# Performance work log

Measured on AMD Instinct MI355X. Metric: run time of the kernel, lower is better.

Reference implementation:

```python
import jax, jax.numpy as jnp
import numpy as np
from jax import lax

B, S, D, H, HFF, T = 256, 33, 42, 128, 256, 20
BN_EPS = 1e-5

def _bn(x, g, b):
    # eval-mode BatchNorm1d with running_mean=0, running_var=1
    return x * (g / jnp.sqrt(1.0 + BN_EPS)) + b

def _gelu(x):
    return jax.nn.gelu(x, approximate=False)  # torch default GELU (exact)

def setup_inputs() -> dict:
    key = jax.random.key(0)
    ks = iter(jax.random.split(key, 48))
    w = lambda shp, s=0.02: jax.random.normal(next(ks), shp, dtype=jnp.float32) * s
    z = lambda shp: jnp.zeros(shp, jnp.float32)
    o = lambda shp: jnp.ones(shp, jnp.float32)
    inp = {
        'interaction_path': jax.random.normal(next(ks), (B, S, D), dtype=jnp.float32),
        'timestamps': jnp.broadcast_to(jnp.arange(S, dtype=jnp.float32) * 0.1, (B, S)),
        # initial encoder: Linear(42->128), BN, GELU, Linear(128->128), BN
        'enc_w1': w((D, H)), 'enc_b1': z(H), 'enc_g1': o(H), 'enc_be1': z(H),
        'enc_w2': w((H, H)), 'enc_b2': z(H), 'enc_g2': o(H), 'enc_be2': z(H),
        # vector field: 128->256 (BN,GELU), 256->256 (BN,GELU) x2, 256->5376
        'vf_w0': w((H, HFF)), 'vf_b0': z(HFF), 'vf_g0': o(HFF), 'vf_be0': z(HFF),
        'vf_w1': w((HFF, HFF)), 'vf_b1': z(HFF), 'vf_g1': o(HFF), 'vf_be1': z(HFF),
        'vf_w2': w((HFF, HFF)), 'vf_b2': z(HFF), 'vf_g2': o(HFF), 'vf_be2': z(HFF),
        'vf_w3': w((HFF, H * D)), 'vf_b3': z(H * D),
        # multihead attention (seq_len = 1 -> softmax is identically 1)
        'wv': w((H, H)), 'bv': z(H), 'wo': w((H, H)), 'bo': z(H),
        # 20 trait decoders, stacked: 128->64->32->1
        'dw1': w((T, H, 64)), 'db1': z((T, 64)),
        'dw2': w((T, 64, 32)), 'db2': z((T, 32)),
        'dw3': w((T, 32, 1)), 'db3': z((T, 1)),
    }
    return inp

def reference(interaction_path, timestamps,
              enc_w1, enc_b1, enc_g1, enc_be1, enc_w2, enc_b2, enc_g2, enc_be2,
              vf_w0, vf_b0, vf_g0, vf_be0, vf_w1, vf_b1, vf_g1, vf_be1,
              vf_w2, vf_b2, vf_g2, vf_be2, vf_w3, vf_b3,
              wv, bv, wo, bo,
              dw1, db1, dw2, db2, dw3, db3):
    b = interaction_path.shape[0]
    # ---- initial encoder on X[:, 0] ----
    x0 = interaction_path[:, 0]                      # [B, D]
    h = _gelu(_bn(x0 @ enc_w1 + enc_b1, enc_g1, enc_be1))
    z0 = _bn(h @ enc_w2 + enc_b2, enc_g2, enc_be2)   # [B, H]

    # ---- CDE vector field: z -> [B, H, D] ----
    def vf(zz):
        y = _gelu(_bn(zz @ vf_w0 + vf_b0, vf_g0, vf_be0))
        y = _gelu(_bn(y @ vf_w1 + vf_b1, vf_g1, vf_be1))
        y = _gelu(_bn(y @ vf_w2 + vf_b2, vf_g2, vf_be2))
        return (y @ vf_w3 + vf_b3).reshape(b, H, D)

    def g(zz, dxdt):  # f(z) @ dX/dt  -> [B, H]
        return jnp.einsum('bhd,bd->bh', vf(zz), dxdt)

    # linear-interpolation control path: piecewise-constant derivative
    t = timestamps[0]                                # [S]
    dt = t[1:] - t[:-1]                              # [S-1]
    dX = interaction_path[:, 1:] - interaction_path[:, :-1]   # [B, S-1, D]
    dXdt = dX / dt[None, :, None]                    # [B, S-1, D]

    def step(zz, x):
        dxdt, hstep = x
        k1 = g(zz, dxdt)
        k2 = g(zz + 0.5 * hstep * k1, dxdt)
        k3 = g(zz + 0.5 * hstep * k2, dxdt)
        k4 = g(zz + hstep * k3, dxdt)
        return zz + (hstep / 6.0) * (k1 + 2.0 * k2 + 2.0 * k3 + k4), None

    zT, _ = lax.scan(step, z0, (jnp.swapaxes(dXdt, 0, 1), dt))  # [B, H]

    # ---- self-attention over a length-1 sequence: softmax==1 -> out_proj(v) ----
    attended = (zT @ wv + bv) @ wo + bo              # [B, H]

    # ---- 20 trait decoders (stacked / vectorized) ----
    h1 = _gelu(jnp.einsum('bh,thd->tbd', attended, dw1) + db1[:, None, :])
    h2 = _gelu(jnp.einsum('tbd,tde->tbe', h1, dw2) + db2[:, None, :])
    out = jax.nn.sigmoid(jnp.einsum('tbe,teo->tbo', h2, dw3) + db3[:, None, :])
    return jnp.transpose(out[..., 0], (1, 0))        # [B, 20]
```

## Files before the change

kernel.cpp:

```cpp
#include <hip/hip_runtime.h>
#include <cstdint>

constexpr int B    = 256;
constexpr int S    = 33;
constexpr int D    = 42;
constexpr int H    = 128;
constexpr int HFF  = 256;
constexpr int T    = 20;
constexpr int NSTEP = S - 1;
constexpr int DP   = D / 2;
constexpr int ADW  = 8192;
constexpr int CH   = 16;
constexpr int NCH  = NSTEP / CH;
#define BN_SCALE 0.9999950000374997f

typedef _Float16 h2v __attribute__((ext_vector_type(2)));
typedef _Float16 f16x8 __attribute__((ext_vector_type(8)));
typedef float    f32x4 __attribute__((ext_vector_type(4)));
union UH2 { uint32_t u; h2v h; };

__device__ __forceinline__ float fdot2u(uint32_t a, uint32_t b, float c) {
    UH2 x, y; x.u = a; y.u = b;
    return __builtin_amdgcn_fdot2(x.h, y.h, c, false);
}
__device__ __forceinline__ uint32_t packh2(float a, float b) {
    UH2 u; u.h = h2v{(_Float16)a, (_Float16)b}; return u.u;
}
__device__ __forceinline__ float gelu_exact(float x) {
    return 0.5f * x * (1.0f + erff(x * 0.70710678118654752f));
}
__device__ __forceinline__ float gelu_fast(float x) {
    float inner = x * (1.0f + 0.044715f * x * x);
    float E = __expf(1.5957691216f * inner);
    return x * E * __frcp_rn(E + 1.0f);
}
__device__ __forceinline__ int aswz(int idx) {
    return (idx & ~31) | ((idx & 31) ^ (((idx >> 9) & 3) << 1));
}

__global__ void __launch_bounds__(256) packprep_kernel(
    const float* __restrict__ w0, const float* __restrict__ w1,
    const float* __restrict__ w2, const float* __restrict__ w3,
    uint32_t* __restrict__ wcol, uint32_t* __restrict__ wp,
    const float* __restrict__ path, const float* __restrict__ ts,
    const float* __restrict__ ew1, const float* __restrict__ eb1,
    const float* __restrict__ eg1, const float* __restrict__ ebe1,
    const float* __restrict__ ew2, const float* __restrict__ eb2,
    const float* __restrict__ eg2, const float* __restrict__ ebe2,
    const float* __restrict__ b3,
    float* __restrict__ zbuf, uint32_t* __restrict__ dxp,
    float* __restrict__ bd3g, float* __restrict__ dtb) {
    int tid = threadIdx.x;
    if (blockIdx.x < 4096) {
        int idx = blockIdx.x * 256 + tid;
        if (idx < 160 * 512) {
            int r = idx >> 9, t = idx & 511;
            int j = t >> 1, half = t & 1;
            float a, bb;
            if (r < 32)      { int ip = half * 32 + r;      a = w0[(2*ip)*HFF + j]; bb = w0[(2*ip+1)*HFF + j]; }
            else if (r < 96) { int ip = half * 64 + (r-32); a = w1[(2*ip)*HFF + j]; bb = w1[(2*ip+1)*HFF + j]; }
            else             { int ip = half * 64 + (r-96); a = w2[(2*ip)*HFF + j]; bb = w2[(2*ip+1)*HFF + j]; }
            wcol[idx] = packh2(a, bb);
        }
        if (idx < 32768 * 32) {
            int m = idx >> 5, dd = (idx & 31) * 2;
            int e = 4 * (m >> 9) + (m & 3);
            int h = (m >> 2) & 127;
            const float* row = w3 + (size_t)e * (H * D) + h * D;
            float a = (dd     < D) ? row[dd]     : 0.f;
            float b = (dd + 1 < D) ? row[dd + 1] : 0.f;
            wp[idx] = packh2(a, b);
        }
        return;
    }
    __shared__ float x0[D], hb[H], dxs[NSTEP][D];
    int b = blockIdx.x - 4096;
    if (tid < D) x0[tid] = path[b * S * D + tid];
    __syncthreads();
    if (tid < H) {
        float acc = eb1[tid];
        for (int d = 0; d < D; ++d) acc += x0[d] * ew1[d * H + tid];
        hb[tid] = gelu_exact(acc * (eg1[tid] * BN_SCALE) + ebe1[tid]);
    }
    __syncthreads();
    if (tid < H) {
        float acc = eb2[tid];
        for (int i = 0; i < H; ++i) acc += hb[i] * ew2[i * H + tid];
        zbuf[b * H + tid] = acc * (eg2[tid] * BN_SCALE) + ebe2[tid];
    }
    for (int idx = tid; idx < NSTEP * 32; idx += 256) {
        int s = idx >> 5, j2 = idx & 31;
        uint32_t val = 0;
        if (j2 < DP) {
            float dtv = ts[s + 1] - ts[s];
            int base = b * S * D + s * D + 2 * j2;
            float v0 = (path[base + D] - path[base]) / dtv;
            float v1 = (path[base + D + 1] - path[base + 1]) / dtv;
            dxs[s][2 * j2] = v0; dxs[s][2 * j2 + 1] = v1;
            val = packh2(v0, v1);
        }
        dxp[((size_t)(s * B + b)) * 32 + j2] = val;
    }
    __syncthreads();
    if (tid < H) {
        for (int s = 0; s < NSTEP; ++s) {
            float a = 0.f;
            for (int d = 0; d < D; ++d) a += b3[tid * D + d] * dxs[s][d];
            bd3g[(size_t)(s * B + b) * H + tid] = a;
        }
    }
    if (b == 0 && tid < NSTEP) dtb[tid] = ts[tid + 1] - ts[tid];
}

__global__ void __launch_bounds__(256) amm_kernel(
    const uint32_t* __restrict__ wp, const uint32_t* __restrict__ dxp,
    uint32_t* __restrict__ Ach, int s0) {
    __shared__ __align__(16) uint32_t xpose[4][16 * 36];
    int t = threadIdx.x;
    int l = t & 63, wid = t >> 6;
    int mg = (blockIdx.x & 63) * 4 + wid;
    int sg = blockIdx.x >> 6;
    int lr = l & 15, lk = l >> 4;
    const char* wpB = (const char*)wp;
    const char* dxB = (const char*)dxp + (size_t)s0 * B * 128;
    char* asB = (char*)Ach;
    uint32_t* xp = xpose[wid];
    f16x8 af0[8], af1[8];
#pragma unroll
    for (int mi = 0; mi < 8; ++mi) {
        const f16x8* p = (const f16x8*)(wpB + ((size_t)(mg * 8 + mi) * 16 + lr) * 128 + lk * 16);
        af0[mi] = p[0]; af1[mi] = p[4];
    }
#pragma unroll
    for (int si = 0; si < 8; ++si) {
        int q = sg * 128 + si * 16 + lr;
#pragma unroll
        for (int mi = 0; mi < 8; ++mi) {
            const f16x8* bp = (const f16x8*)(dxB + (size_t)q * 128 + lk * 16);
            f16x8 b0 = bp[0], b1 = bp[4];
            f32x4 acc = {0.f, 0.f, 0.f, 0.f};
            acc = __builtin_amdgcn_mfma_f32_16x16x32_f16(af0[mi], b0, acc, 0, 0, 0);
            acc = __builtin_amdgcn_mfma_f32_16x16x32_f16(af1[mi], b1, acc, 0, 0, 0);
            uint32_t P0 = packh2(acc[0], acc[1]) + 0x00800080u;
            uint32_t P1 = packh2(acc[2], acc[3]) + 0x00800080u;
            uint32_t Q = __builtin_amdgcn_perm(P1, P0, 0x07050301u);
            xp[lr * 36 + lk + 4 * mi] = Q;
        }
        __syncthreads();
        {
            int qr = l >> 2, seg = l & 3;
            const uint4* src = (const uint4*)(xp + qr * 36 + seg * 8);
            uint4 v0 = src[0], v1 = src[1];
            int qout = sg * 128 + si * 16 + qr;
            char* outB = asB + (size_t)qout * 32768 + mg * 128 + seg * 32;
            *(uint4*)outB = v0;
            *(uint4*)(outB + 16) = v1;
        }
        __syncthreads();
    }
}

__global__ void __launch_bounds__(512, 1)
__attribute__((amdgpu_waves_per_eu(2, 8)))
scan_kernel(
    const uint32_t* __restrict__ wcol, const uint32_t* __restrict__ Ach,
    const float* __restrict__ vb0, const float* __restrict__ vg0, const float* __restrict__ vbe0,
    const float* __restrict__ vb1, const float* __restrict__ vg1, const float* __restrict__ vbe1,
    const float* __restrict__ vb2, const float* __restrict__ vg2, const float* __restrict__ vbe2,
    const float* __restrict__ bd3g, const float* __restrict__ dtb,
    float* __restrict__ zbuf, int s0, int do_att,
    const float* __restrict__ wv, const float* __restrict__ bv,
    const float* __restrict__ wo, const float* __restrict__ bo,
    float* __restrict__ att) {
    __shared__ __align__(16) uint32_t ABUF[2][ADW];
    __shared__ __align__(16) uint32_t zzPd[72];
    __shared__ __align__(16) uint32_t yA[136], yB[136], yC[136];
    int t = threadIdx.x, b = blockIdx.x;
    int j = t >> 1, half = t & 1;
    int h = t >> 2, g = t & 3;
    int hswz = h ^ (g << 3);
    uint32_t w0h[32], w1h[64], w2h[64];
#pragma unroll
    for (int r = 0; r < 32; ++r) w0h[r] = wcol[r * 512 + t];
#pragma unroll
    for (int r = 0; r < 64; ++r) w1h[r] = wcol[(32 + r) * 512 + t];
#pragma unroll
    for (int r = 0; r < 64; ++r) w2h[r] = wcol[(96 + r) * 512 + t];
    float c0s = vg0[j] * BN_SCALE, c0o = vb0[j] * c0s + vbe0[j];
    float c1s = vg1[j] * BN_SCALE, c1o = vb1[j] * c1s + vbe1[j];
    float c2s = vg2[j] * BN_SCALE, c2o = vb2[j] * c2s + vbe2[j];
    float zf = zbuf[b * H + h];
    {
        const uint4* Ag = (const uint4*)(Ach + (size_t)b * ADW);
        uint4 a0 = Ag[t], a1 = Ag[512 + t], a2 = Ag[1024 + t], a3 = Ag[1536 + t];
        uint4* Ad = (uint4*)ABUF[0];
        Ad[aswz(t)] = a0; Ad[aswz(512 + t)] = a1;
        Ad[aswz(1024 + t)] = a2; Ad[aswz(1536 + t)] = a3;
    }
    {
        float zhi = __shfl_down(zf, 4, 64);
        if ((t & 7) == 0) {
            int ip = t >> 3;
            zzPd[(ip >> 5) * 36 + (ip & 31)] = packh2(zf, zhi);
        }
    }
    __syncthreads();

    for (int sl = 0; sl < CH; ++sl) {
        int s = s0 + sl;
        float hstep = dtb[s];
        float bd3 = bd3g[(size_t)(s * B + b) * H + h];
        uint4 pf0, pf1, pf2, pf3;
        {
            int sn = (sl + 1 < CH) ? sl + 1 : sl;
            const uint4* Ag = (const uint4*)(Ach + (size_t)(sn * B + b) * ADW);
            pf0 = Ag[t]; pf1 = Ag[512 + t]; pf2 = Ag[1024 + t]; pf3 = Ag[1536 + t];
        }
        const uint32_t* AL = ABUF[sl & 1];
        float ksum = 0.f, kcur = 0.f;
        for (int r = 0; r < 4; ++r) {
            {
                float pa = 0.f, pb = 0.f, pc = 0.f, pd = 0.f;
                const uint4* zq = (const uint4*)(zzPd + half * 36);
#pragma unroll
                for (int u4 = 0; u4 < 8; ++u4) {
                    uint4 zv = zq[u4];
                    pa = fdot2u(w0h[4*u4+0], zv.x, pa); pb = fdot2u(w0h[4*u4+1], zv.y, pb);
                    pc = fdot2u(w0h[4*u4+2], zv.z, pc); pd = fdot2u(w0h[4*u4+3], zv.w, pd);
                }
                float p = (pa + pb) + (pc + pd);
                p += __shfl_xor(p, 1, 64);
                float v = gelu_fast(p * c0s + c0o);
                float vhi = __shfl_down(v, 2, 64);
                if ((t & 3) == 0) {
                    int ip = t >> 2;
                    yA[(ip >> 6) * 68 + (ip & 63)] = packh2(v, vhi);
                }
            }
            __syncthreads();
            {
                float pa = 0.f, pb = 0.f, pc = 0.f, pd = 0.f;
                const uint4* yq = (const uint4*)(yA + half * 68);
#pragma unroll
                for (int u4 = 0; u4 < 16; ++u4) {
                    uint4 yv = yq[u4];
                    pa = fdot2u(w1h[4*u4+0], yv.x, pa); pb = fdot2u(w1h[4*u4+1], yv.y, pb);
                    pc = fdot2u(w1h[4*u4+2], yv.z, pc); pd = fdot2u(w1h[4*u4+3], yv.w, pd);
                }
                float p = (pa + pb) + (pc + pd);
                p += __shfl_xor(p, 1, 64);
                float v = gelu_fast(p * c1s + c1o);
                float vhi = __shfl_down(v, 2, 64);
                if ((t & 3) == 0) {
                    int ip = t >> 2;
                    yB[(ip >> 6) * 68 + (ip & 63)] = packh2(v, vhi);
                }
            }
            __syncthreads();
            {
                float pa = 0.f, pb = 0.f, pc = 0.f, pd = 0.f;
                const uint4* yq = (const uint4*)(yB + half * 68);
#pragma unroll
                for (int u4 = 0; u4 < 16; ++u4) {
                    uint4 yv = yq[u4];
                    pa = fdot2u(w2h[4*u4+0], yv.x, pa); pb = fdot2u(w2h[4*u4+1], yv.y, pb);
                    pc = fdot2u(w2h[4*u4+2], yv.z, pc); pd = fdot2u(w2h[4*u4+3], yv.w, pd);
                }
                float p = (pa + pb) + (pc + pd);
                p += __shfl_xor(p, 1, 64);
                float v = gelu_fast(p * c2s + c2o);
                float vhi = __shfl_down(v, 2, 64);
                if ((t & 3) == 0) {
                    int ip = t >> 2;
                    yC[(ip >> 6) * 68 + (ip & 63)] = packh2(v, vhi);
                }
            }
            __syncthreads();
            {
                float pA = 0.f, pB = 0.f, pC = 0.f, pD = 0.f;
                int ybase = (g >> 1) * 68 + (g & 1) * 32;
                const uint4* yq = (const uint4*)(yC + ybase);
#pragma unroll
                for (int kk = 0; kk < 8; ++kk) {
                    uint4 yv = yq[kk];
                    int k0 = g * 16 + 2 * kk;
                    uint32_t Qa = AL[k0 * 128 + hswz];
                    uint32_t Qb = AL[(k0 + 1) * 128 + hswz];
                    pA = fdot2u(__builtin_amdgcn_perm(0u, Qa, 0x010C000Cu), yv.x, pA);
                    pB = fdot2u(__builtin_amdgcn_perm(0u, Qa, 0x030C020Cu), yv.y, pB);
                    pC = fdot2u(__builtin_amdgcn_perm(0u, Qb, 0x010C000Cu), yv.z, pC);
                    pD = fdot2u(__builtin_amdgcn_perm(0u, Qb, 0x030C020Cu), yv.w, pD);
                }
                float ptot = (pA + pB) + (pC + pD);
                ptot += __shfl_xor(ptot, 1, 64);
                ptot += __shfl_xor(ptot, 2, 64);
                kcur = bd3 + ptot;
                float wsm = (r == 1 || r == 2) ? 2.f : 1.f;
                ksum += wsm * kcur;
                float zz;
                if (r < 3) {
                    float cin = (r == 2) ? 1.f : 0.5f;
                    zz = zf + cin * hstep * kcur;
                } else {
                    zf += hstep * (1.f / 6.f) * ksum;
                    zz = zf;
                }
                float zhi = __shfl_down(zz, 4, 64);
                if ((t & 7) == 0) {
                    int ip = t >> 3;
                    zzPd[(ip >> 5) * 36 + (ip & 31)] = packh2(zz, zhi);
                }
            }
            if (r == 3) {
                uint4* Ad = (uint4*)ABUF[(sl + 1) & 1];
                Ad[aswz(t)] = pf0; Ad[aswz(512 + t)] = pf1;
                Ad[aswz(1024 + t)] = pf2; Ad[aswz(1536 + t)] = pf3;
            }
            __syncthreads();
        }
    }
    if ((t & 3) == 0) zbuf[b * H + h] = zf;
    if (do_att) {
        float* zfl = (float*)ABUF[0];
        float* vv  = zfl + 128;
        if ((t & 3) == 0) zfl[h] = zf;
        __syncthreads();
        {
            float acc = 0.f;
            int i0 = 32 * g;
#pragma unroll 8
            for (int i = 0; i < 32; ++i) {
                int ii = i0 + ((i + 8 * g) & 31);
                acc += zfl[ii] * wv[ii * H + h];
            }
            acc += __shfl_xor(acc, 1, 64);
            acc += __shfl_xor(acc, 2, 64);
            if (g == 0) vv[h] = acc + bv[h];
        }
        __syncthreads();
        {
            float acc = 0.f;
            int i0 = 32 * g;
#pragma unroll 8
            for (int i = 0; i < 32; ++i) {
                int ii = i0 + ((i + 8 * g) & 31);
                acc += vv[ii] * wo[ii * H + h];
            }
            acc += __shfl_xor(acc, 1, 64);
            acc += __shfl_xor(acc, 2, 64);
            if (g == 0) att[b * H + h] = acc + bo[h];
        }
    }
}

__global__ void __launch_bounds__(64) dec_kernel(
    const float* __restrict__ att,
    const float* __restrict__ dw1, const float* __restrict__ db1,
    const float* __restrict__ dw2, const float* __restrict__ db2,
    const float* __restrict__ dw3, const float* __restrict__ db3,
    float* __restrict__ out) {
    int bid = blockIdx.x;
    int t = bid >> 8, b = bid & 255;
    int tid = threadIdx.x;
    __shared__ float al[H], h1l[64];
    al[tid] = att[b * H + tid];
    al[tid + 64] = att[b * H + tid + 64];
    __syncthreads();
    {
        float acc = db1[t * 64 + tid];
#pragma unroll 8
        for (int i = 0; i < H; ++i) acc += al[i] * dw1[t * H * 64 + i * 64 + tid];
        h1l[tid] = gelu_exact(acc);
    }
    __syncthreads();
    float v = 0.f;
    if (tid < 32) {
        float acc = db2[t * 32 + tid];
#pragma unroll 8
        for (int i = 0; i < 64; ++i) acc += h1l[i] * dw2[t * 64 * 32 + i * 32 + tid];
        v = gelu_exact(acc) * dw3[t * 32 + tid];
    }
#pragma unroll
    for (int off = 16; off >= 1; off >>= 1) v += __shfl_down(v, off, 64);
    if (tid == 0) out[b * T + t] = 1.f / (1.f + expf(-(v + db3[t])));
}

extern "C" void kernel_launch(void* const* d_in, const int* in_sizes, int n_in,
                              void* d_out, int out_size, void* d_ws, size_t ws_size,
                              hipStream_t stream) {
    const float* path = (const float*)d_in[0];
    const float* ts   = (const float*)d_in[1];
    const float* ew1  = (const float*)d_in[2];
    const float* eb1  = (const float*)d_in[3];
    const float* eg1  = (const float*)d_in[4];
    const float* ebe1 = (const float*)d_in[5];
    const float* ew2  = (const float*)d_in[6];
    const float* eb2  = (const float*)d_in[7];
    const float* eg2  = (const float*)d_in[8];
    const float* ebe2 = (const float*)d_in[9];
    const float* vw0  = (const float*)d_in[10];
    const float* vb0  = (const float*)d_in[11];
    const float* vg0  = (const float*)d_in[12];
    const float* vbe0 = (const float*)d_in[13];
    const float* vw1  = (const float*)d_in[14];
    const float* vb1  = (const float*)d_in[15];
    const float* vg1  = (const float*)d_in[16];
    const float* vbe1 = (const float*)d_in[17];
    const float* vw2  = (const float*)d_in[18];
    const float* vb2  = (const float*)d_in[19];
    const float* vg2  = (const float*)d_in[20];
    const float* vbe2 = (const float*)d_in[21];
    const float* vw3  = (const float*)d_in[22];
    const float* vb3  = (const float*)d_in[23];
    const float* wv   = (const float*)d_in[24];
    const float* bv   = (const float*)d_in[25];
    const float* wo   = (const float*)d_in[26];
    const float* bo   = (const float*)d_in[27];
    const float* dw1  = (const float*)d_in[28];
    const float* db1  = (const float*)d_in[29];
    const float* dw2  = (const float*)d_in[30];
    const float* db2  = (const float*)d_in[31];
    const float* dw3  = (const float*)d_in[32];
    const float* db3  = (const float*)d_in[33];

    char* ws = (char*)d_ws;
    size_t off = 0;
    auto take = [&](size_t bytes) { char* p = ws + off; off += (bytes + 255) & ~(size_t)255; return p; };
    uint32_t* Ach   = (uint32_t*)take((size_t)CH * B * ADW * 4);
    uint32_t* dxp   = (uint32_t*)take((size_t)NSTEP * B * 32 * 4);
    float*    bd3g  = (float*)take((size_t)NSTEP * B * H * 4);
    float*    dtb   = (float*)take(NSTEP * 4);
    float*    zbuf  = (float*)take((size_t)B * H * 4);
    float*    att   = (float*)take((size_t)B * H * 4);
    uint32_t* wcol  = (uint32_t*)take((size_t)160 * 512 * 4);
    uint32_t* wp    = (uint32_t*)take((size_t)32768 * 32 * 4);

    packprep_kernel<<<4096 + B, 256, 0, stream>>>(
        vw0, vw1, vw2, vw3, wcol, wp,
        path, ts, ew1, eb1, eg1, ebe1, ew2, eb2, eg2, ebe2, vb3,
        zbuf, dxp, bd3g, dtb);
    for (int c = 0; c < NCH; ++c) {
        amm_kernel<<<2048, 256, 0, stream>>>(wp, dxp, Ach, c * CH);
        scan_kernel<<<B, 512, 0, stream>>>(wcol, Ach,
                                           vb0, vg0, vbe0, vb1, vg1, vbe1, vb2, vg2, vbe2,
                                           bd3g, dtb, zbuf, c * CH,
                                           (c == NCH - 1) ? 1 : 0,
                                           wv, bv, wo, bo, att);
    }
    dec_kernel<<<T * B, 64, 0, stream>>>(att, dw1, db1, dw2, db2, dw3, db3, (float*)d_out);
}
```

Before: 532.5 us.

## Overlap next-chunk A-matrix GEMM with scan via fused double-buffered kernel

New measurement: 567.5 us. +6.6%, slower.

```diff
diff --git a/kernel.cpp b/kernel.cpp
--- a/kernel.cpp
+++ b/kernel.cpp
@@ -10,7 +10,7 @@
 constexpr int NSTEP = S - 1;
 constexpr int DP   = D / 2;
 constexpr int ADW  = 8192;
-constexpr int CH   = 16;
+constexpr int CH   = 8;
 constexpr int NCH  = NSTEP / CH;
 #define BN_SCALE 0.9999950000374997f
 
@@ -160,22 +160,74 @@
     }
 }
 
+template<int MODE>
 __global__ void __launch_bounds__(512, 1)
 __attribute__((amdgpu_waves_per_eu(2, 8)))
-scan_kernel(
-    const uint32_t* __restrict__ wcol, const uint32_t* __restrict__ Ach,
+scanx_kernel(
+    const uint32_t* __restrict__ wcol, const uint32_t* __restrict__ AchR,
+    uint32_t* __restrict__ AchW,
+    const uint32_t* __restrict__ wp, const uint32_t* __restrict__ dxp,
     const float* __restrict__ vb0, const float* __restrict__ vg0, const float* __restrict__ vbe0,
     const float* __restrict__ vb1, const float* __restrict__ vg1, const float* __restrict__ vbe1,
     const float* __restrict__ vb2, const float* __restrict__ vg2, const float* __restrict__ vbe2,
     const float* __restrict__ bd3g, const float* __restrict__ dtb,
-    float* __restrict__ zbuf, int s0, int do_att,
+    float* __restrict__ zbuf, int s0, int s0_amm,
     const float* __restrict__ wv, const float* __restrict__ bv,
     const float* __restrict__ wo, const float* __restrict__ bo,
     float* __restrict__ att) {
     __shared__ __align__(16) uint32_t ABUF[2][ADW];
     __shared__ __align__(16) uint32_t zzPd[72];
     __shared__ __align__(16) uint32_t yA[136], yB[136], yC[136];
-    int t = threadIdx.x, b = blockIdx.x;
+    int t = threadIdx.x;
+
+    if (MODE == 0 && blockIdx.x >= B) {
+        int rid = blockIdx.x - B;
+        int wid = t >> 6, l = t & 63;
+        int w = rid * 8 + wid;
+        int mg = w & 255, sg = w >> 8;
+        int lr = l & 15, lk = l >> 4;
+        const char* wpB = (const char*)wp;
+        const char* dxB = (const char*)dxp + (size_t)s0_amm * B * 128;
+        char* asB = (char*)AchW;
+        uint32_t* xp = (uint32_t*)ABUF[0] + wid * (16 * 36);
+        f16x8 af0[8], af1[8];
+#pragma unroll
+        for (int mi = 0; mi < 8; ++mi) {
+            const f16x8* p = (const f16x8*)(wpB + ((size_t)(mg * 8 + mi) * 16 + lr) * 128 + lk * 16);
+            af0[mi] = p[0]; af1[mi] = p[4];
+        }
+#pragma unroll
+        for (int si = 0; si < 8; ++si) {
+            int q = sg * 128 + si * 16 + lr;
+#pragma unroll
+            for (int mi = 0; mi < 8; ++mi) {
+                const f16x8* bp = (const f16x8*)(dxB + (size_t)q * 128 + lk * 16);
+                f16x8 b0 = bp[0], b1 = bp[4];
+                f32x4 acc = {0.f, 0.f, 0.f, 0.f};
+                acc = __builtin_amdgcn_mfma_f32_16x16x32_f16(af0[mi], b0, acc, 0, 0, 0);
+                acc = __builtin_amdgcn_mfma_f32_16x16x32_f16(af1[mi], b1, acc, 0, 0, 0);
+                uint32_t P0 = packh2(acc[0], acc[1]) + 0x00800080u;
+                uint32_t P1 = packh2(acc[2], acc[3]) + 0x00800080u;
+                uint32_t Q = __builtin_amdgcn_perm(P1, P0, 0x07050301u);
+                xp[lr * 36 + lk + 4 * mi] = Q;
+            }
+            __syncthreads();
+            {
+                int qr = l >> 2, seg = l & 3;
+                const uint4* src = (const uint4*)(xp + qr * 36 + seg * 8);
+                uint4 v0 = src[0], v1 = src[1];
+                int qout = sg * 128 + si * 16 + qr;
+                char* outB = asB + (size_t)qout * 32768 + mg * 128 + seg * 32;
+                *(uint4*)outB = v0;
+                *(uint4*)(outB + 16) = v1;
+            }
+            __syncthreads();
+        }
+        return;
+    }
+
+    __builtin_amdgcn_s_setprio(1);
+    int b = blockIdx.x;
     int j = t >> 1, half = t & 1;
     int h = t >> 2, g = t & 3;
     int hswz = h ^ (g << 3);
@@ -191,7 +243,7 @@
     float c2s = vg2[j] * BN_SCALE, c2o = vb2[j] * c2s + vbe2[j];
     float zf = zbuf[b * H + h];
     {
-        const uint4* Ag = (const uint4*)(Ach + (size_t)b * ADW);
+        const uint4* Ag = (const uint4*)(AchR + (size_t)b * ADW);
         uint4 a0 = Ag[t], a1 = Ag[512 + t], a2 = Ag[1024 + t], a3 = Ag[1536 + t];
         uint4* Ad = (uint4*)ABUF[0];
         Ad[aswz(t)] = a0; Ad[aswz(512 + t)] = a1;
@@ -213,7 +265,7 @@
         uint4 pf0, pf1, pf2, pf3;
         {
             int sn = (sl + 1 < CH) ? sl + 1 : sl;
-            const uint4* Ag = (const uint4*)(Ach + (size_t)(sn * B + b) * ADW);
+            const uint4* Ag = (const uint4*)(AchR + (size_t)(sn * B + b) * ADW);
             pf0 = Ag[t]; pf1 = Ag[512 + t]; pf2 = Ag[1024 + t]; pf3 = Ag[1536 + t];
         }
         const uint32_t* AL = ABUF[sl & 1];
@@ -320,7 +372,7 @@
         }
     }
     if ((t & 3) == 0) zbuf[b * H + h] = zf;
-    if (do_att) {
+    if (MODE == 1) {
         float* zfl = (float*)ABUF[0];
         float* vv  = zfl + 128;
         if ((t & 3) == 0) zfl[h] = zf;
@@ -426,7 +478,8 @@
     char* ws = (char*)d_ws;
     size_t off = 0;
     auto take = [&](size_t bytes) { char* p = ws + off; off += (bytes + 255) & ~(size_t)255; return p; };
-    uint32_t* Ach   = (uint32_t*)take((size_t)CH * B * ADW * 4);
+    uint32_t* Ach0  = (uint32_t*)take((size_t)CH * B * ADW * 4);
+    uint32_t* Ach1  = (uint32_t*)take((size_t)CH * B * ADW * 4);
     uint32_t* dxp   = (uint32_t*)take((size_t)NSTEP * B * 32 * 4);
     float*    bd3g  = (float*)take((size_t)NSTEP * B * H * 4);
     float*    dtb   = (float*)take(NSTEP * 4);
@@ -434,18 +487,27 @@
     float*    att   = (float*)take((size_t)B * H * 4);
     uint32_t* wcol  = (uint32_t*)take((size_t)160 * 512 * 4);
     uint32_t* wp    = (uint32_t*)take((size_t)32768 * 32 * 4);
+    uint32_t* AchB[2] = { Ach0, Ach1 };
 
     packprep_kernel<<<4096 + B, 256, 0, stream>>>(
         vw0, vw1, vw2, vw3, wcol, wp,
         path, ts, ew1, eb1, eg1, ebe1, ew2, eb2, eg2, ebe2, vb3,
         zbuf, dxp, bd3g, dtb);
+    amm_kernel<<<1024, 256, 0, stream>>>(wp, dxp, AchB[0], 0);
     for (int c = 0; c < NCH; ++c) {
-        amm_kernel<<<2048, 256, 0, stream>>>(wp, dxp, Ach, c * CH);
-        scan_kernel<<<B, 512, 0, stream>>>(wcol, Ach,
-                                           vb0, vg0, vbe0, vb1, vg1, vbe1, vb2, vg2, vbe2,
-                                           bd3g, dtb, zbuf, c * CH,
-                                           (c == NCH - 1) ? 1 : 0,
-                                           wv, bv, wo, bo, att);
+        if (c < NCH - 1) {
+            scanx_kernel<0><<<B + 512, 512, 0, stream>>>(
+                wcol, AchB[c & 1], AchB[(c + 1) & 1], wp, dxp,
+                vb0, vg0, vbe0, vb1, vg1, vbe1, vb2, vg2, vbe2,
+                bd3g, dtb, zbuf, c * CH, (c + 1) * CH,
+                wv, bv, wo, bo, att);
+        } else {
+            scanx_kernel<1><<<B, 512, 0, stream>>>(
+                wcol, AchB[c & 1], AchB[c & 1], wp, dxp,
+                vb0, vg0, vbe0, vb1, vg1, vbe1, vb2, vg2, vbe2,
+                bd3g, dtb, zbuf, c * CH, 0,
+                wv, bv, wo, bo, att);
+        }
     }
     dec_kernel<<<T * B, 64, 0, stream>>>(att, dw1, db1, dw2, db2, dw3, db3, (float*)d_out);
 }
```
